# Performance work log

Hardware: AMD Instinct MI355X
Metric: run time of the kernel (lower is better)

Reference implementation:

```python
import jax, jax.numpy as jnp
import numpy as np

SCALE = 100.0  # sharp-softmax temperature from the torch module

def _build_tables():
    # ByteToNibbleFFN: W1 is identity(256) so it is mathematically a no-op; keep W2.
    W2_b2n = np.zeros((256, 32), np.float32)
    bb = np.arange(256)
    W2_b2n[bb, bb >> 4] = 1.0
    W2_b2n[bb, 16 + (bb & 15)] = 1.0
    # NibbleAddWithCarryFFN tables
    W1_add = np.zeros((34, 512), np.float32)
    W2_sum = np.zeros((512, 16), np.float32)
    W2_cout = np.zeros((512, 2), np.float32)
    for a in range(16):
        for b in range(16):
            for c in range(2):
                idx = a * 32 + b * 2 + c
                W1_add[a, idx] = 1.0
                W1_add[16 + b, idx] = 1.0
                W1_add[32 + c, idx] = 1.0
                t = a + b + c
                W2_sum[idx, t & 15] = 1.0
                W2_cout[idx, 1 if t > 15 else 0] = 1.0
    # NibbleToByteFFN tables
    W1_n2b = np.zeros((32, 256), np.float32)
    W2_n2b = np.zeros((256, 256), np.float32)
    for h in range(16):
        for l in range(16):
            addr = h * 16 + l
            W1_n2b[h, addr] = 1.0
            W1_n2b[16 + l, addr] = 1.0
            W2_n2b[addr, (h << 4) | l] = 1.0
    return tuple(jnp.asarray(t) for t in (W2_b2n, W1_add, W2_sum, W2_cout, W1_n2b, W2_n2b))

W2_B2N, W1_ADD, W2_SUM, W2_COUT, W1_N2B, W2_N2B = _build_tables()

def _b2n(x):
    # byte [.,256] -> (high [.,16], low [.,16]); W1=eye(256) omitted (identity)
    out = x @ W2_B2N
    return out[..., :16], out[..., 16:]

def _nib_add(a, b, cin):
    combined = jnp.concatenate([a, b, cin], axis=-1)           # [.,34]
    address = jax.nn.softmax(combined @ W1_ADD * SCALE, axis=-1)  # [.,512]
    return address @ W2_SUM, address @ W2_COUT

def _n2b(high, low):
    combined = jnp.concatenate([high, low], axis=-1)           # [.,32]
    address = jax.nn.softmax(combined @ W1_N2B * SCALE, axis=-1)  # [.,256]
    return address @ W2_N2B

def setup_inputs() -> dict:
    key = jax.random.key(0)
    k1, k2 = jax.random.split(key)
    B = 32768
    a = jax.random.uniform(k1, (B, 4, 256), dtype=jnp.float32)
    b = jax.random.uniform(k2, (B, 4, 256), dtype=jnp.float32)
    return {"a": a, "b": b}

def reference(a, b):
    # NeuralALU.add: ripple-carry add over 4 bytes, 2 nibble adds per byte
    B = a.shape[0]
    carry = jnp.zeros((B, 2), a.dtype).at[:, 0].set(1.0)  # carry_zero one-hot
    out_bytes = []
    for i in range(4):  # fixed structural loop over bytes (carry dependence)
        ah, al = _b2n(a[:, i])
        bh, bl = _b2n(b[:, i])
        sl, carry = _nib_add(al, bl, carry)
        sh, carry = _nib_add(ah, bh, carry)
        out_bytes.append(_n2b(sh, sl))
    return jnp.stack(out_bytes, axis=1)  # [B,4,256]
```

## Files before the change

kernel.cpp:

```cpp
#include <hip/hip_runtime.h>

#define NIB_SCALE 100.0f

typedef float vfloat4 __attribute__((ext_vector_type(4)));

template<int CTRL>
__device__ __forceinline__ float fdpp(float x) {
    return __int_as_float(__builtin_amdgcn_update_dpp(
        0, __float_as_int(x), CTRL, 0xF, 0xF, true));
}

__device__ __forceinline__ float rsum16d(float v) {
    v += fdpp<0x121>(v); v += fdpp<0x122>(v); v += fdpp<0x124>(v); v += fdpp<0x128>(v);
    return v;
}
__device__ __forceinline__ float rmax16d(float v) {
    v = fmaxf(v, fdpp<0x121>(v)); v = fmaxf(v, fdpp<0x122>(v));
    v = fmaxf(v, fdpp<0x124>(v)); v = fmaxf(v, fdpp<0x128>(v));
    return v;
}
__device__ __forceinline__ float scan16d(float v) {
    v += fdpp<0x111>(v); v += fdpp<0x112>(v); v += fdpp<0x114>(v); v += fdpp<0x118>(v);
    return v;
}
__device__ __forceinline__ float softmax16d(float v) {
    float m = rmax16d(v);
    float e = __expf(NIB_SCALE * (v - m));
    float s = rsum16d(e);
    return e / s;
}
__device__ __forceinline__ float sharp_sigmoid(float c) {
    return 1.0f / (1.0f + __expf(NIB_SCALE * (1.0f - 2.0f * c)));
}

#define GATHER_ROT(dst, src)            \
    dst[0]  = (src);                    \
    dst[1]  = fdpp<0x121>(src);         \
    dst[2]  = fdpp<0x122>(src);         \
    dst[3]  = fdpp<0x123>(src);         \
    dst[4]  = fdpp<0x124>(src);         \
    dst[5]  = fdpp<0x125>(src);         \
    dst[6]  = fdpp<0x126>(src);         \
    dst[7]  = fdpp<0x127>(src);         \
    dst[8]  = fdpp<0x128>(src);         \
    dst[9]  = fdpp<0x129>(src);         \
    dst[10] = fdpp<0x12A>(src);         \
    dst[11] = fdpp<0x12B>(src);         \
    dst[12] = fdpp<0x12C>(src);         \
    dst[13] = fdpp<0x12D>(src);         \
    dst[14] = fdpp<0x12E>(src);         \
    dst[15] = fdpp<0x12F>(src);

#define COLSUM_CHUNK(dst, r4, c)                                  \
    {                                                             \
        float s0 = rsum16d(r4.x), s1 = rsum16d(r4.y);             \
        float s2 = rsum16d(r4.z), s3 = rsum16d(r4.w);             \
        float t0 = (k & 1) ? s1 : s0;                             \
        float t1 = (k & 1) ? s3 : s2;                             \
        float tc = (k & 2) ? t1 : t0;                             \
        dst = ((k >> 2) == (c)) ? tc : dst;                       \
    }

__global__ __launch_bounds__(256) void nalu_kernel(const float* __restrict__ A,
                                                   const float* __restrict__ B,
                                                   float* __restrict__ O,
                                                   int nrows) {
    __shared__ __align__(16) float sQL[16][16];
    __shared__ __align__(16) float sQH[16][16];
    __shared__ __align__(16) float sPSL[16][16];
    __shared__ __align__(16) float sPSH[16][16];
    __shared__ __align__(16) float sOV[4][4][4];

    const int tid = threadIdx.x;
    const int k = tid & 15;
    const int g = tid >> 4;
    const int b = g & 3;
    const int w = tid >> 6;
    const int row = blockIdx.x * 4 + w;
    if (row >= nrows) return;
    const long base = (long)row * 1024 + b * 256;

    const float4* pa4 = (const float4*)(A + base + 16 * k);
    const float4* pb4 = (const float4*)(B + base + 16 * k);
    float4 ra0 = pa4[0], ra1 = pa4[1], ra2 = pa4[2], ra3 = pa4[3];
    float4 rb0 = pb4[0], rb1 = pb4[1], rb2 = pb4[2], rb3 = pb4[3];

    float ah = ((ra0.x + ra0.y) + (ra0.z + ra0.w)) + ((ra1.x + ra1.y) + (ra1.z + ra1.w))
             + ((ra2.x + ra2.y) + (ra2.z + ra2.w)) + ((ra3.x + ra3.y) + (ra3.z + ra3.w));
    float bh = ((rb0.x + rb0.y) + (rb0.z + rb0.w)) + ((rb1.x + rb1.y) + (rb1.z + rb1.w))
             + ((rb2.x + rb2.y) + (rb2.z + rb2.w)) + ((rb3.x + rb3.y) + (rb3.z + rb3.w));

    float al = 0.f, bl = 0.f;
    COLSUM_CHUNK(al, ra0, 0) COLSUM_CHUNK(al, ra1, 1)
    COLSUM_CHUNK(al, ra2, 2) COLSUM_CHUNK(al, ra3, 3)
    COLSUM_CHUNK(bl, rb0, 0) COLSUM_CHUNK(bl, rb1, 1)
    COLSUM_CHUNK(bl, rb2, 2) COLSUM_CHUNK(bl, rb3, 3)

    float pal = softmax16d(al);
    float pbl = softmax16d(bl);
    float pah = softmax16d(ah);
    float pbh = softmax16d(bh);

    sQL[g][k] = pbl;
    sQH[g][k] = pbh;

    float mirl = fdpp<0x140>(pbl);
    float mirh = fdpp<0x140>(pbh);
    float T15l = scan16d(mirl);
    float T15h = scan16d(mirh);
    float ov15l = rsum16d(pal * T15l);
    float c15l  = rsum16d(pal * mirl);
    float ov15h = rsum16d(pah * T15h);
    float c15h  = rsum16d(pah * mirh);
    float ov16l = ov15l - c15l;
    float ov16h = ov15h - c15h;

    sOV[w][0][b] = ov16l;
    sOV[w][1][b] = ov15l;
    sOV[w][2][b] = ov16h;
    sOV[w][3][b] = ov15h;

    float QL[16], QH[16];
    *(float4*)&QL[0]  = *(const float4*)&sQL[g][0];
    *(float4*)&QL[4]  = *(const float4*)&sQL[g][4];
    *(float4*)&QL[8]  = *(const float4*)&sQL[g][8];
    *(float4*)&QL[12] = *(const float4*)&sQL[g][12];
    float GL[16];
    GATHER_ROT(GL, pal)
    float rl = 0.f;
    #pragma unroll
    for (int j = 0; j < 16; ++j) rl = fmaf(GL[j], QL[j], rl);

    *(float4*)&QH[0]  = *(const float4*)&sQH[g][0];
    *(float4*)&QH[4]  = *(const float4*)&sQH[g][4];
    *(float4*)&QH[8]  = *(const float4*)&sQH[g][8];
    *(float4*)&QH[12] = *(const float4*)&sQH[g][12];
    float GH[16];
    GATHER_ROT(GH, pah)
    float rh = 0.f;
    #pragma unroll
    for (int j = 0; j < 16; ++j) rh = fmaf(GH[j], QH[j], rh);

    float4 O16L = *(const float4*)&sOV[w][0][0];
    float4 O15L = *(const float4*)&sOV[w][1][0];
    float4 O16H = *(const float4*)&sOV[w][2][0];
    float4 O15H = *(const float4*)&sOV[w][3][0];

    float qc1_0 = sharp_sigmoid(O16L.x);
    float qc0_0 = 1.f - qc1_0;
    float pc1_1 = sharp_sigmoid(qc0_0 * O16H.x + qc1_0 * O15H.x);
    float pc0_1 = 1.f - pc1_1;
    float qc1_1 = sharp_sigmoid(pc0_1 * O16L.y + pc1_1 * O15L.y);
    float qc0_1 = 1.f - qc1_1;
    float pc1_2 = sharp_sigmoid(qc0_1 * O16H.y + qc1_1 * O15H.y);
    float pc0_2 = 1.f - pc1_2;
    float qc1_2 = sharp_sigmoid(pc0_2 * O16L.z + pc1_2 * O15L.z);
    float qc0_2 = 1.f - qc1_2;
    float pc1_3 = sharp_sigmoid(qc0_2 * O16H.z + qc1_2 * O15H.z);
    float pc0_3 = 1.f - pc1_3;
    float qc1_3 = sharp_sigmoid(pc0_3 * O16L.w + pc1_3 * O15L.w);
    float qc0_3 = 1.f - qc1_3;

    float pc0 = b == 0 ? 1.f   : b == 1 ? pc0_1 : b == 2 ? pc0_2 : pc0_3;
    float pc1 = b == 0 ? 0.f   : b == 1 ? pc1_1 : b == 2 ? pc1_2 : pc1_3;
    float qc0 = b == 0 ? qc0_0 : b == 1 ? qc0_1 : b == 2 ? qc0_2 : qc0_3;
    float qc1 = b == 0 ? qc1_0 : b == 1 ? qc1_1 : b == 2 ? qc1_2 : qc1_3;

    float slow  = pc0 * rl + pc1 * fdpp<0x121>(rl);
    float shigh = qc0 * rh + qc1 * fdpp<0x121>(rh);

    float psl = softmax16d(slow);
    float psh = softmax16d(shigh);
    sPSL[g][k] = psl;
    sPSH[g][k] = psh;

    float4 pslq = *(const float4*)&sPSL[g][4 * (k & 3)];
    float* po = O + base;
    #pragma unroll
    for (int c = 0; c < 4; ++c) {
        float hs = sPSH[g][4 * c + (k >> 2)];
        vfloat4 o4;
        o4.x = hs * pslq.x; o4.y = hs * pslq.y; o4.z = hs * pslq.z; o4.w = hs * pslq.w;
        __builtin_nontemporal_store(o4, (vfloat4*)(po + 64 * c + 4 * k));
    }
}

extern "C" void kernel_launch(void* const* d_in, const int* in_sizes, int n_in,
                              void* d_out, int out_size, void* d_ws, size_t ws_size,
                              hipStream_t stream) {
    const float* A = (const float*)d_in[0];
    const float* B = (const float*)d_in[1];
    float* O = (float*)d_out;
    int nrows = in_sizes[0] / 1024;
    int grid = (nrows + 3) / 4;
    nalu_kernel<<<grid, 256, 0, stream>>>(A, B, O, nrows);
}
```

Baseline: 316.9 us.

## Process four rows per wave with register double-buffered prefetch of next row

Each wave now loops over four rows instead of one and loads the next row's A/B data into registers while computing the current row. This is meant to hide global load latency through software pipelining and to cut the grid size by four. It also swaps the nontemporal output stores for plain stores and drops the launch_bounds attribute, which raises register pressure and lowers the number of resident blocks.

```diff
diff --git a/kernel.cpp b/kernel.cpp
--- a/kernel.cpp
+++ b/kernel.cpp
@@ -1,8 +1,6 @@
 #include <hip/hip_runtime.h>
 
 #define NIB_SCALE 100.0f
-
-typedef float vfloat4 __attribute__((ext_vector_type(4)));
 
 template<int CTRL>
 __device__ __forceinline__ float fdpp(float x) {
@@ -33,23 +31,10 @@
     return 1.0f / (1.0f + __expf(NIB_SCALE * (1.0f - 2.0f * c)));
 }
 
-#define GATHER_ROT(dst, src)            \
-    dst[0]  = (src);                    \
-    dst[1]  = fdpp<0x121>(src);         \
-    dst[2]  = fdpp<0x122>(src);         \
-    dst[3]  = fdpp<0x123>(src);         \
-    dst[4]  = fdpp<0x124>(src);         \
-    dst[5]  = fdpp<0x125>(src);         \
-    dst[6]  = fdpp<0x126>(src);         \
-    dst[7]  = fdpp<0x127>(src);         \
-    dst[8]  = fdpp<0x128>(src);         \
-    dst[9]  = fdpp<0x129>(src);         \
-    dst[10] = fdpp<0x12A>(src);         \
-    dst[11] = fdpp<0x12B>(src);         \
-    dst[12] = fdpp<0x12C>(src);         \
-    dst[13] = fdpp<0x12D>(src);         \
-    dst[14] = fdpp<0x12E>(src);         \
-    dst[15] = fdpp<0x12F>(src);
+__device__ __forceinline__ float conv_quad(float g0, float g1, float g2, float g3,
+                                           const float4 q) {
+    return fmaf(g0, q.x, fmaf(g1, q.y, fmaf(g2, q.z, g3 * q.w)));
+}
 
 #define COLSUM_CHUNK(dst, r4, c)                                  \
     {                                                             \
@@ -61,91 +46,9 @@
         dst = ((k >> 2) == (c)) ? tc : dst;                       \
     }
 
-__global__ __launch_bounds__(256) void nalu_kernel(const float* __restrict__ A,
-                                                   const float* __restrict__ B,
-                                                   float* __restrict__ O,
-                                                   int nrows) {
-    __shared__ __align__(16) float sQL[16][16];
-    __shared__ __align__(16) float sQH[16][16];
-    __shared__ __align__(16) float sPSL[16][16];
-    __shared__ __align__(16) float sPSH[16][16];
-    __shared__ __align__(16) float sOV[4][4][4];
-
-    const int tid = threadIdx.x;
-    const int k = tid & 15;
-    const int g = tid >> 4;
-    const int b = g & 3;
-    const int w = tid >> 6;
-    const int row = blockIdx.x * 4 + w;
-    if (row >= nrows) return;
-    const long base = (long)row * 1024 + b * 256;
-
-    const float4* pa4 = (const float4*)(A + base + 16 * k);
-    const float4* pb4 = (const float4*)(B + base + 16 * k);
-    float4 ra0 = pa4[0], ra1 = pa4[1], ra2 = pa4[2], ra3 = pa4[3];
-    float4 rb0 = pb4[0], rb1 = pb4[1], rb2 = pb4[2], rb3 = pb4[3];
-
-    float ah = ((ra0.x + ra0.y) + (ra0.z + ra0.w)) + ((ra1.x + ra1.y) + (ra1.z + ra1.w))
-             + ((ra2.x + ra2.y) + (ra2.z + ra2.w)) + ((ra3.x + ra3.y) + (ra3.z + ra3.w));
-    float bh = ((rb0.x + rb0.y) + (rb0.z + rb0.w)) + ((rb1.x + rb1.y) + (rb1.z + rb1.w))
-             + ((rb2.x + rb2.y) + (rb2.z + rb2.w)) + ((rb3.x + rb3.y) + (rb3.z + rb3.w));
-
-    float al = 0.f, bl = 0.f;
-    COLSUM_CHUNK(al, ra0, 0) COLSUM_CHUNK(al, ra1, 1)
-    COLSUM_CHUNK(al, ra2, 2) COLSUM_CHUNK(al, ra3, 3)
-    COLSUM_CHUNK(bl, rb0, 0) COLSUM_CHUNK(bl, rb1, 1)
-    COLSUM_CHUNK(bl, rb2, 2) COLSUM_CHUNK(bl, rb3, 3)
-
-    float pal = softmax16d(al);
-    float pbl = softmax16d(bl);
-    float pah = softmax16d(ah);
-    float pbh = softmax16d(bh);
-
-    sQL[g][k] = pbl;
-    sQH[g][k] = pbh;
-
-    float mirl = fdpp<0x140>(pbl);
-    float mirh = fdpp<0x140>(pbh);
-    float T15l = scan16d(mirl);
-    float T15h = scan16d(mirh);
-    float ov15l = rsum16d(pal * T15l);
-    float c15l  = rsum16d(pal * mirl);
-    float ov15h = rsum16d(pah * T15h);
-    float c15h  = rsum16d(pah * mirh);
-    float ov16l = ov15l - c15l;
-    float ov16h = ov15h - c15h;
-
-    sOV[w][0][b] = ov16l;
-    sOV[w][1][b] = ov15l;
-    sOV[w][2][b] = ov16h;
-    sOV[w][3][b] = ov15h;
-
-    float QL[16], QH[16];
-    *(float4*)&QL[0]  = *(const float4*)&sQL[g][0];
-    *(float4*)&QL[4]  = *(const float4*)&sQL[g][4];
-    *(float4*)&QL[8]  = *(const float4*)&sQL[g][8];
-    *(float4*)&QL[12] = *(const float4*)&sQL[g][12];
-    float GL[16];
-    GATHER_ROT(GL, pal)
-    float rl = 0.f;
-    #pragma unroll
-    for (int j = 0; j < 16; ++j) rl = fmaf(GL[j], QL[j], rl);
-
-    *(float4*)&QH[0]  = *(const float4*)&sQH[g][0];
-    *(float4*)&QH[4]  = *(const float4*)&sQH[g][4];
-    *(float4*)&QH[8]  = *(const float4*)&sQH[g][8];
-    *(float4*)&QH[12] = *(const float4*)&sQH[g][12];
-    float GH[16];
-    GATHER_ROT(GH, pah)
-    float rh = 0.f;
-    #pragma unroll
-    for (int j = 0; j < 16; ++j) rh = fmaf(GH[j], QH[j], rh);
-
-    float4 O16L = *(const float4*)&sOV[w][0][0];
-    float4 O15L = *(const float4*)&sOV[w][1][0];
-    float4 O16H = *(const float4*)&sOV[w][2][0];
-    float4 O15H = *(const float4*)&sOV[w][3][0];
-
+__device__ __forceinline__ void carry_chain(const float4 O16L, const float4 O15L,
+                                            const float4 O16H, const float4 O15H, int b,
+                                            float& pc0, float& pc1, float& qc0, float& qc1) {
     float qc1_0 = sharp_sigmoid(O16L.x);
     float qc0_0 = 1.f - qc1_0;
     float pc1_1 = sharp_sigmoid(qc0_0 * O16H.x + qc1_0 * O15H.x);
@@ -160,28 +63,125 @@
     float pc0_3 = 1.f - pc1_3;
     float qc1_3 = sharp_sigmoid(pc0_3 * O16L.w + pc1_3 * O15L.w);
     float qc0_3 = 1.f - qc1_3;
+    pc0 = b == 0 ? 1.f   : b == 1 ? pc0_1 : b == 2 ? pc0_2 : pc0_3;
+    pc1 = b == 0 ? 0.f   : b == 1 ? pc1_1 : b == 2 ? pc1_2 : pc1_3;
+    qc0 = b == 0 ? qc0_0 : b == 1 ? qc0_1 : b == 2 ? qc0_2 : qc0_3;
+    qc1 = b == 0 ? qc1_0 : b == 1 ? qc1_1 : b == 2 ? qc1_2 : qc1_3;
+}
 
-    float pc0 = b == 0 ? 1.f   : b == 1 ? pc0_1 : b == 2 ? pc0_2 : pc0_3;
-    float pc1 = b == 0 ? 0.f   : b == 1 ? pc1_1 : b == 2 ? pc1_2 : pc1_3;
-    float qc0 = b == 0 ? qc0_0 : b == 1 ? qc0_1 : b == 2 ? qc0_2 : qc0_3;
-    float qc1 = b == 0 ? qc1_0 : b == 1 ? qc1_1 : b == 2 ? qc1_2 : qc1_3;
+__global__ void nalu_kernel(const float* __restrict__ A,
+                            const float* __restrict__ B,
+                            float* __restrict__ O,
+                            int nrows) {
+    __shared__ __align__(16) float sQL[16][16];
+    __shared__ __align__(16) float sQH[16][16];
+    __shared__ __align__(16) float sPSL[16][16];
+    __shared__ __align__(16) float sPSH[16][16];
+    __shared__ __align__(16) float sOV[4][4][4];
 
-    float slow  = pc0 * rl + pc1 * fdpp<0x121>(rl);
-    float shigh = qc0 * rh + qc1 * fdpp<0x121>(rh);
+    const int tid = threadIdx.x;
+    const int k = tid & 15;
+    const int g = tid >> 4;
+    const int b = g & 3;
+    const int w = tid >> 6;
+    constexpr int ROWS = 4;
+    const int row0 = blockIdx.x * (4 * ROWS) + w * ROWS;
+    if (row0 >= nrows) return;
+    long base = (long)row0 * 1024 + b * 256;
 
-    float psl = softmax16d(slow);
-    float psh = softmax16d(shigh);
-    sPSL[g][k] = psl;
-    sPSH[g][k] = psh;
+    const float4* pa4 = (const float4*)(A + base + 16 * k);
+    const float4* pb4 = (const float4*)(B + base + 16 * k);
+    float4 ra0 = pa4[0], ra1 = pa4[1], ra2 = pa4[2], ra3 = pa4[3];
+    float4 rb0 = pb4[0], rb1 = pb4[1], rb2 = pb4[2], rb3 = pb4[3];
 
-    float4 pslq = *(const float4*)&sPSL[g][4 * (k & 3)];
-    float* po = O + base;
     #pragma unroll
-    for (int c = 0; c < 4; ++c) {
-        float hs = sPSH[g][4 * c + (k >> 2)];
-        vfloat4 o4;
-        o4.x = hs * pslq.x; o4.y = hs * pslq.y; o4.z = hs * pslq.z; o4.w = hs * pslq.w;
-        __builtin_nontemporal_store(o4, (vfloat4*)(po + 64 * c + 4 * k));
+    for (int i = 0; i < ROWS; ++i) {
+        if (row0 + i >= nrows) break;
+        const bool more = (i + 1 < ROWS) && (row0 + i + 1 < nrows);
+        const long nbase = more ? base + 1024 : base;
+
+        const float4* na4 = (const float4*)(A + nbase + 16 * k);
+        const float4* nb4 = (const float4*)(B + nbase + 16 * k);
+        float4 xa0 = na4[0], xa1 = na4[1], xa2 = na4[2], xa3 = na4[3];
+        float4 xb0 = nb4[0], xb1 = nb4[1], xb2 = nb4[2], xb3 = nb4[3];
+
+        float ah = ((ra0.x + ra0.y) + (ra0.z + ra0.w)) + ((ra1.x + ra1.y) + (ra1.z + ra1.w))
+                 + ((ra2.x + ra2.y) + (ra2.z + ra2.w)) + ((ra3.x + ra3.y) + (ra3.z + ra3.w));
+        float bh = ((rb0.x + rb0.y) + (rb0.z + rb0.w)) + ((rb1.x + rb1.y) + (rb1.z + rb1.w))
+                 + ((rb2.x + rb2.y) + (rb2.z + rb2.w)) + ((rb3.x + rb3.y) + (rb3.z + rb3.w));
+        float al = 0.f, bl = 0.f;
+        COLSUM_CHUNK(al, ra0, 0) COLSUM_CHUNK(al, ra1, 1)
+        COLSUM_CHUNK(al, ra2, 2) COLSUM_CHUNK(al, ra3, 3)
+        COLSUM_CHUNK(bl, rb0, 0) COLSUM_CHUNK(bl, rb1, 1)
+        COLSUM_CHUNK(bl, rb2, 2) COLSUM_CHUNK(bl, rb3, 3)
+
+        __builtin_amdgcn_sched_barrier(0);
+
+        float pal = softmax16d(al);
+        float pbl = softmax16d(bl);
+        float pah = softmax16d(ah);
+        float pbh = softmax16d(bh);
+
+        sQL[g][k] = pbl;
+        sQH[g][k] = pbh;
+
+        float mirl = fdpp<0x140>(pbl);
+        float mirh = fdpp<0x140>(pbh);
+        float T15l = scan16d(mirl);
+        float T15h = scan16d(mirh);
+        float ov15l = rsum16d(pal * T15l);
+        float c15l  = rsum16d(pal * mirl);
+        float ov15h = rsum16d(pah * T15h);
+        float c15h  = rsum16d(pah * mirh);
+
+        sOV[w][0][b] = ov15l - c15l;
+        sOV[w][1][b] = ov15l;
+        sOV[w][2][b] = ov15h - c15h;
+        sOV[w][3][b] = ov15h;
+
+        const float4 La = *(const float4*)&sQL[g][0];
+        const float4 Lb = *(const float4*)&sQL[g][4];
+        const float4 Lc = *(const float4*)&sQL[g][8];
+        const float4 Ld = *(const float4*)&sQL[g][12];
+        float rl = (conv_quad(pal,              fdpp<0x121>(pal), fdpp<0x122>(pal), fdpp<0x123>(pal), La)
+                  + conv_quad(fdpp<0x124>(pal), fdpp<0x125>(pal), fdpp<0x126>(pal), fdpp<0x127>(pal), Lb))
+                 + (conv_quad(fdpp<0x128>(pal), fdpp<0x129>(pal), fdpp<0x12A>(pal), fdpp<0x12B>(pal), Lc)
+                  + conv_quad(fdpp<0x12C>(pal), fdpp<0x12D>(pal), fdpp<0x12E>(pal), fdpp<0x12F>(pal), Ld));
+
+        const float4 Ha = *(const float4*)&sQH[g][0];
+        const float4 Hb = *(const float4*)&sQH[g][4];
+        const float4 Hc = *(const float4*)&sQH[g][8];
+        const float4 Hd = *(const float4*)&sQH[g][12];
+        float rh = (conv_quad(pah,              fdpp<0x121>(pah), fdpp<0x122>(pah), fdpp<0x123>(pah), Ha)
+                  + conv_quad(fdpp<0x124>(pah), fdpp<0x125>(pah), fdpp<0x126>(pah), fdpp<0x127>(pah), Hb))
+                 + (conv_quad(fdpp<0x128>(pah), fdpp<0x129>(pah), fdpp<0x12A>(pah), fdpp<0x12B>(pah), Hc)
+                  + conv_quad(fdpp<0x12C>(pah), fdpp<0x12D>(pah), fdpp<0x12E>(pah), fdpp<0x12F>(pah), Hd));
+
+        float pc0, pc1, qc0, qc1;
+        carry_chain(*(const float4*)&sOV[w][0][0], *(const float4*)&sOV[w][1][0],
+                    *(const float4*)&sOV[w][2][0], *(const float4*)&sOV[w][3][0],
+                    b, pc0, pc1, qc0, qc1);
+
+        float slow  = pc0 * rl + pc1 * fdpp<0x121>(rl);
+        float shigh = qc0 * rh + qc1 * fdpp<0x121>(rh);
+
+        float psl = softmax16d(slow);
+        float psh = softmax16d(shigh);
+        sPSL[g][k] = psl;
+        sPSH[g][k] = psh;
+
+        const float4 pslq = *(const float4*)&sPSL[g][4 * (k & 3)];
+        float* po = O + base;
+        #pragma unroll
+        for (int c = 0; c < 4; ++c) {
+            float hs = sPSH[g][4 * c + (k >> 2)];
+            *(float4*)(po + 64 * c + 4 * k) =
+                make_float4(hs * pslq.x, hs * pslq.y, hs * pslq.z, hs * pslq.w);
+        }
+
+        ra0 = xa0; ra1 = xa1; ra2 = xa2; ra3 = xa3;
+        rb0 = xb0; rb1 = xb1; rb2 = xb2; rb3 = xb3;
+        base = nbase;
     }
 }
 
@@ -192,6 +192,6 @@
     const float* B = (const float*)d_in[1];
     float* O = (float*)d_out;
     int nrows = in_sizes[0] / 1024;
-    int grid = (nrows + 3) / 4;
+    int grid = (nrows + 15) / 16;
     nalu_kernel<<<grid, 256, 0, stream>>>(A, B, O, nrows);
 }
```

New measurement: 315.1 us. Within noise of the previous version (-0.6%).
